# Optimization experiments

Hardware: AMD Instinct MI355X
Metric: run time of the kernel (lower is better)

## Reference

```python
import jax, jax.numpy as jnp
import numpy as np

B, NQ, NV = 4, 16384, 16384
DIM, FRAMES = 64, 4
D = DIM * FRAMES            # embed_dims = 256
HEADS, POINTS, LEVELS = 8, 4, 1
HD = D // HEADS             # head_dim = 32
HL, WL = 128, 128           # single-level feature map, HL*WL == NV
EPS = 1e-6


def setup_inputs() -> dict:
    key = jax.random.key(0)
    ks = jax.random.split(key, 14)
    inp = {
        "query": jax.random.normal(ks[0], (B, NQ, D), jnp.float32),
        "feat": jax.random.normal(ks[1], (B, NV, D), jnp.float32),
        "reference_points": jax.random.uniform(ks[2], (B, NQ, LEVELS, 2), jnp.float32),
        "spatial_shapes": jnp.array([[HL, WL]], jnp.int32),
        "level_start_index": jnp.array([0], jnp.int32),
        # LayerNorm params
        "qn_scale": jnp.ones((D,), jnp.float32),
        "qn_bias": jnp.zeros((D,), jnp.float32),
        "fn_scale": jnp.ones((D,), jnp.float32),
        "fn_bias": jnp.zeros((D,), jnp.float32),
        # MSDeformAttn projections
        "W_value": jax.random.normal(ks[3], (D, D), jnp.float32) / np.sqrt(D),
        "b_value": jnp.zeros((D,), jnp.float32),
        "W_off": jax.random.normal(ks[4], (D, HEADS * LEVELS * POINTS * 2), jnp.float32) * 0.01,
        "b_off": jax.random.normal(ks[5], (HEADS * LEVELS * POINTS * 2,), jnp.float32) * 0.5,
        "W_attn": jax.random.normal(ks[6], (D, HEADS * LEVELS * POINTS), jnp.float32) * 0.02,
        "b_attn": jnp.zeros((HEADS * LEVELS * POINTS,), jnp.float32),
        "W_out": jax.random.normal(ks[7], (D, D), jnp.float32) / np.sqrt(D),
        "b_out": jnp.zeros((D,), jnp.float32),
        # gamma is a learned scale (init 0 in the module; randomized here so it contributes)
        "gamma": jax.random.normal(ks[8], (D,), jnp.float32) * 0.1,
    }
    return inp


def _layer_norm(x, scale, bias):
    mu = jnp.mean(x, axis=-1, keepdims=True)
    var = jnp.mean(jnp.square(x - mu), axis=-1, keepdims=True)
    return (x - mu) * jax.lax.rsqrt(var + EPS) * scale + bias


def _bilinear_gather(v, loc, Hl, Wl):
    # v:   [B, H, N, hd] flattened level values (row-major HxW)
    # loc: [B, H, NQ, P, 2] normalized sampling locations in [0,1]
    # grid_sample semantics: align_corners=False, zero padding
    x = loc[..., 0] * Wl - 0.5
    y = loc[..., 1] * Hl - 0.5
    x0 = jnp.floor(x); y0 = jnp.floor(y)
    x1 = x0 + 1.0;     y1 = y0 + 1.0
    wx1 = x - x0; wx0 = 1.0 - wx1
    wy1 = y - y0; wy0 = 1.0 - wy1
    out = 0.0
    for xi, yi, w in ((x0, y0, wx0 * wy0), (x1, y0, wx1 * wy0),
                      (x0, y1, wx0 * wy1), (x1, y1, wx1 * wy1)):
        inb = (xi >= 0) & (xi < Wl) & (yi >= 0) & (yi < Hl)
        idx = (jnp.clip(yi, 0, Hl - 1) * Wl + jnp.clip(xi, 0, Wl - 1)).astype(jnp.int32)
        Bc, Hc, NQc, Pc = idx.shape
        g = jnp.take_along_axis(v, idx.reshape(Bc, Hc, NQc * Pc)[..., None], axis=2)
        g = g.reshape(Bc, Hc, NQc, Pc, -1)          # [B, H, NQ, P, hd]
        out = out + g * (w * inb)[..., None]
    return out


def reference(query, feat, reference_points, spatial_shapes, level_start_index,
              qn_scale, qn_bias, fn_scale, fn_bias,
              W_value, b_value, W_off, b_off, W_attn, b_attn, W_out, b_out, gamma):
    Bq, nq, _ = query.shape
    q = _layer_norm(query, qn_scale, qn_bias)
    v = _layer_norm(feat, fn_scale, fn_bias)

    # value projection -> per-head values [B, H, NV, hd]
    value = (v @ W_value + b_value).reshape(Bq, -1, HEADS, HD).transpose(0, 2, 1, 3)

    # sampling offsets [B, NQ, H, L, P, 2] and attention weights (softmax over L*P)
    off = (q @ W_off + b_off).reshape(Bq, nq, HEADS, LEVELS, POINTS, 2)
    aw = jax.nn.softmax((q @ W_attn + b_attn).reshape(Bq, nq, HEADS, LEVELS * POINTS), axis=-1)
    aw = aw.reshape(Bq, nq, HEADS, LEVELS, POINTS)

    ss = np.asarray(spatial_shapes)          # static level geometry
    lsi = np.asarray(level_start_index)
    offset_norm = ss[:, ::-1].astype(np.float32)  # (W, H) per level
    # sampling locations [B, NQ, H, L, P, 2]
    loc = reference_points[:, :, None, :, None, :] + off / offset_norm[None, None, None, :, None, :]

    acc = jnp.zeros((Bq, HEADS, nq, HD), query.dtype)
    for l in range(LEVELS):
        Hl, Wl = int(ss[l, 0]), int(ss[l, 1])
        start = int(lsi[l])
        v_l = value[:, :, start:start + Hl * Wl]                # [B, H, Hl*Wl, hd]
        loc_l = loc[:, :, :, l].transpose(0, 2, 1, 3, 4)        # [B, H, NQ, P, 2]
        sampled = _bilinear_gather(v_l, loc_l, Hl, Wl)          # [B, H, NQ, P, hd]
        aw_l = aw[:, :, :, l].transpose(0, 2, 1, 3)             # [B, H, NQ, P]
        acc = acc + jnp.einsum('bhnpd,bhnp->bhnd', sampled, aw_l)

    out = acc.transpose(0, 2, 1, 3).reshape(Bq, nq, D) @ W_out + b_out
    return query + gamma * out
```

## Files before the change

### kernel.cpp

```cpp
#include <hip/hip_runtime.h>

#define NQ 16384
#define NV 16384
#define DMODEL 256

typedef __bf16 bf16x8 __attribute__((ext_vector_type(8)));
typedef float f32x4 __attribute__((ext_vector_type(4)));

__device__ __forceinline__ unsigned short f2bf(float x) {
    union { float f; unsigned int u; } v; v.f = x;
    unsigned int r = v.u + 0x7fff + ((v.u >> 16) & 1);
    return (unsigned short)(r >> 16);
}
__device__ __forceinline__ float blo(unsigned int u) {
    union { unsigned int u; float f; } v; v.u = u << 16; return v.f;
}
__device__ __forceinline__ float bhi(unsigned int u) {
    union { unsigned int u; float f; } v; v.u = u & 0xFFFF0000u; return v.f;
}
__device__ __forceinline__ f32x4 mfma16(bf16x8 a, bf16x8 b, f32x4 c) {
    return __builtin_amdgcn_mfma_f32_16x16x32_bf16(a, b, c, 0, 0, 0);
}

__global__ __launch_bounds__(256) void k_prep(
    const float* __restrict__ Wv, const float* __restrict__ Woff,
    const float* __restrict__ Wattn, const float* __restrict__ Wout,
    unsigned short* __restrict__ WtV, unsigned short* __restrict__ WtC,
    unsigned short* __restrict__ WtO) {
    int t = blockIdx.x * 256 + threadIdx.x;
    if (t < 256 * 256) { int n = t >> 8, k = t & 255; WtV[t] = f2bf(Wv[k * 256 + n]); return; }
    t -= 256 * 256;
    if (t < 256 * 256) { int n = t >> 8, k = t & 255; WtO[t] = f2bf(Wout[k * 256 + n]); return; }
    t -= 256 * 256;
    if (t < 96 * 256) {
        int j = t >> 8, k = t & 255;
        float w = (j < 64) ? Woff[k * 64 + j] : Wattn[k * 32 + (j - 64)];
        WtC[j * 256 + k] = f2bf(w);
    }
}

__global__ __launch_bounds__(256) void k_ln(
    const float* __restrict__ feat, const float* __restrict__ query,
    const float* __restrict__ fns, const float* __restrict__ fnb,
    const float* __restrict__ qns, const float* __restrict__ qnb,
    unsigned short* __restrict__ lnf, unsigned short* __restrict__ lnq) {
    const int blk = blockIdx.x;
    const float* src; const float* scale; const float* bias; unsigned short* dst;
    int row0;
    if (blk < 2048) { src = feat;  scale = fns; bias = fnb; dst = lnf; row0 = blk * 32; }
    else            { src = query; scale = qns; bias = qnb; dst = lnq; row0 = (blk - 2048) * 32; }
    const int lane = threadIdx.x & 63;
    const int w = threadIdx.x >> 6;
    const int g = lane >> 4, li = lane & 15;
    float4 sc[4], bi[4];
#pragma unroll
    for (int j = 0; j < 4; ++j) {
        sc[j] = *(const float4*)(scale + li * 16 + j * 4);
        bi[j] = *(const float4*)(bias + li * 16 + j * 4);
    }
    const int r0 = row0 + w * 8 + g;
    float4 x[2][4];
#pragma unroll
    for (int h2 = 0; h2 < 2; ++h2)
#pragma unroll
        for (int j = 0; j < 4; ++j)
            x[h2][j] = *(const float4*)(src + (size_t)(r0 + h2 * 4) * 256 + li * 16 + j * 4);
#pragma unroll
    for (int h2 = 0; h2 < 2; ++h2) {
        float s = 0.f, sq = 0.f;
#pragma unroll
        for (int j = 0; j < 4; ++j) {
            s  += x[h2][j].x + x[h2][j].y + x[h2][j].z + x[h2][j].w;
            sq += x[h2][j].x * x[h2][j].x + x[h2][j].y * x[h2][j].y +
                  x[h2][j].z * x[h2][j].z + x[h2][j].w * x[h2][j].w;
        }
#pragma unroll
        for (int d = 1; d < 16; d <<= 1) {
            s  += __shfl_xor(s, d);
            sq += __shfl_xor(sq, d);
        }
        float mu = s * 0.00390625f;
        float rstd = rsqrtf(sq * 0.00390625f - mu * mu + 1e-6f);
        unsigned int pk[8];
#pragma unroll
        for (int j = 0; j < 4; ++j) {
            pk[2 * j] = (unsigned)f2bf((x[h2][j].x - mu) * rstd * sc[j].x + bi[j].x) |
                        ((unsigned)f2bf((x[h2][j].y - mu) * rstd * sc[j].y + bi[j].y) << 16);
            pk[2 * j + 1] = (unsigned)f2bf((x[h2][j].z - mu) * rstd * sc[j].z + bi[j].z) |
                            ((unsigned)f2bf((x[h2][j].w - mu) * rstd * sc[j].w + bi[j].w) << 16);
        }
        uint4* dstp = (uint4*)(dst + (size_t)(r0 + h2 * 4) * 256 + li * 16);
        dstp[0] = make_uint4(pk[0], pk[1], pk[2], pk[3]);
        dstp[1] = make_uint4(pk[4], pk[5], pk[6], pk[7]);
    }
}

#define STAGE_A(srcbuf)                                                               \
    {                                                                                 \
        const int c = threadIdx.x & 31;                                               \
        const int rt = threadIdx.x >> 5;                                              \
        _Pragma("unroll") for (int i = 0; i < 16; ++i) {                              \
            const int r = rt + i * 8;                                                 \
            *(uint4*)&A[r * 264 + c * 8] =                                            \
                *(const uint4*)((srcbuf) + (size_t)(m0 + r) * 256 + c * 8);           \
        }                                                                             \
    }

#define MFMA_STEP_V(bf, kk)                                                           \
    _Pragma("unroll") for (int m = 0; m < 8; ++m) {                                   \
        bf16x8 a = *(const bf16x8*)&A[(m * 16 + lrow) * 264 + (kk) * 32 + lk];        \
        _Pragma("unroll") for (int i = 0; i < 4; ++i)                                 \
            acc[i][m] = mfma16(bf[i], a, acc[i][m]);                                  \
    }

__global__ __launch_bounds__(256) void k_value(
    const unsigned short* __restrict__ lnf, const float* __restrict__ b_value,
    const unsigned short* __restrict__ WtV, unsigned short* __restrict__ value) {
    __shared__ unsigned short A[128 * 264];
    const int m0 = blockIdx.x * 128;
    STAGE_A(lnf)
    __syncthreads();
    const int lane = threadIdx.x & 63;
    const int w = threadIdx.x >> 6;
    const int lrow = lane & 15, lk = (lane >> 4) * 8;
    f32x4 acc[4][8];
#pragma unroll
    for (int i = 0; i < 4; ++i)
#pragma unroll
        for (int m = 0; m < 8; ++m) acc[i][m] = (f32x4){0.f, 0.f, 0.f, 0.f};
#define LOADB_V(dst, kk)                                                              \
    _Pragma("unroll") for (int i = 0; i < 4; ++i) dst[i] =                            \
        *(const bf16x8*)(WtV + (size_t)((w * 4 + i) * 16 + lrow) * 256 + (kk) * 32 + lk);
    {
        bf16x8 b0[4], b1[4];
        LOADB_V(b0, 0)
#pragma unroll
        for (int k2 = 0; k2 < 4; ++k2) {
            LOADB_V(b1, k2 * 2 + 1)
            MFMA_STEP_V(b0, k2 * 2)
            if (k2 < 3) { LOADB_V(b0, k2 * 2 + 2) }
            MFMA_STEP_V(b1, k2 * 2 + 1)
        }
    }
    const int g = lane >> 4;
    float4 bv[4];
#pragma unroll
    for (int i = 0; i < 4; ++i) bv[i] = *(const float4*)(b_value + (w * 4 + i) * 16 + g * 4);
#pragma unroll
    for (int m = 0; m < 8; ++m) {
        const size_t row = (size_t)(m0 + m * 16 + (lane & 15));
#pragma unroll
        for (int i = 0; i < 4; ++i) {
            const int col0 = (w * 4 + i) * 16 + g * 4;
            uint2 r;
            r.x = (unsigned)f2bf(acc[i][m][0] + bv[i].x) | ((unsigned)f2bf(acc[i][m][1] + bv[i].y) << 16);
            r.y = (unsigned)f2bf(acc[i][m][2] + bv[i].z) | ((unsigned)f2bf(acc[i][m][3] + bv[i].w) << 16);
            *(uint2*)(value + row * 256 + col0) = r;
        }
    }
}

__global__ __launch_bounds__(256) void k_qoff(
    const unsigned short* __restrict__ lnq, const float* __restrict__ refpt,
    const float* __restrict__ b_off, const float* __restrict__ b_attn,
    const unsigned short* __restrict__ WtC, float4* __restrict__ samples) {
    __shared__ unsigned short A[128 * 264];
    const int m0 = blockIdx.x * 128;
    STAGE_A(lnq)
    __syncthreads();
    const int lane = threadIdx.x & 63;
    const int w = threadIdx.x >> 6;
    const int lrow = lane & 15, lk = (lane >> 4) * 8;
    f32x4 acc[6][2];
#pragma unroll
    for (int i = 0; i < 6; ++i)
#pragma unroll
        for (int m = 0; m < 2; ++m) acc[i][m] = (f32x4){0.f, 0.f, 0.f, 0.f};
#define LOADB_Q(dst, kk)                                                              \
    _Pragma("unroll") for (int i = 0; i < 6; ++i) dst[i] =                            \
        *(const bf16x8*)(WtC + (size_t)(i * 16 + lrow) * 256 + (kk) * 32 + lk);
#define MFMA_STEP_Q(bf, kk)                                                           \
    _Pragma("unroll") for (int m = 0; m < 2; ++m) {                                   \
        bf16x8 a = *(const bf16x8*)&A[(w * 32 + m * 16 + lrow) * 264 + (kk) * 32 + lk]; \
        _Pragma("unroll") for (int i = 0; i < 6; ++i)                                 \
            acc[i][m] = mfma16(bf[i], a, acc[i][m]);                                  \
    }
    {
        bf16x8 b0[6], b1[6];
        LOADB_Q(b0, 0)
#pragma unroll
        for (int k2 = 0; k2 < 4; ++k2) {
            LOADB_Q(b1, k2 * 2 + 1)
            MFMA_STEP_Q(b0, k2 * 2)
            if (k2 < 3) { LOADB_Q(b0, k2 * 2 + 2) }
            MFMA_STEP_Q(b1, k2 * 2 + 1)
        }
    }
    __syncthreads();
    float* Dl = (float*)A + w * 4224;
#pragma unroll
    for (int i = 0; i < 6; ++i) {
        const int col0 = i * 16 + (lane >> 4) * 4;
#pragma unroll
        for (int m = 0; m < 2; ++m) {
            const int rl = m * 16 + (lane & 15);
            *(float4*)&Dl[rl * 100 + col0] =
                make_float4(acc[i][m][0], acc[i][m][1], acc[i][m][2], acc[i][m][3]);
        }
    }
    __syncthreads();
#pragma unroll
    for (int it = 0; it < 4; ++it) {
        int idx = it * 64 + lane;
        int rl = idx >> 3;
        int h = idx & 7;
        int row = m0 + w * 32 + rl;
        float rx = refpt[(size_t)row * 2 + 0] * 128.f - 0.5f;
        float ry = refpt[(size_t)row * 2 + 1] * 128.f - 0.5f;
        float l0 = Dl[rl * 100 + 64 + h * 4 + 0] + b_attn[h * 4 + 0];
        float l1 = Dl[rl * 100 + 64 + h * 4 + 1] + b_attn[h * 4 + 1];
        float l2 = Dl[rl * 100 + 64 + h * 4 + 2] + b_attn[h * 4 + 2];
        float l3 = Dl[rl * 100 + 64 + h * 4 + 3] + b_attn[h * 4 + 3];
        float mx = fmaxf(fmaxf(l0, l1), fmaxf(l2, l3));
        float e0 = __expf(l0 - mx), e1 = __expf(l1 - mx);
        float e2 = __expf(l2 - mx), e3 = __expf(l3 - mx);
        float inv = 1.f / (e0 + e1 + e2 + e3);
        float ww[4] = {e0 * inv, e1 * inv, e2 * inv, e3 * inv};
#pragma unroll
        for (int p = 0; p < 4; ++p) {
            float ox = Dl[rl * 100 + h * 8 + p * 2 + 0] + b_off[h * 8 + p * 2 + 0];
            float oy = Dl[rl * 100 + h * 8 + p * 2 + 1] + b_off[h * 8 + p * 2 + 1];
            samples[((size_t)row * 8 + h) * 4 + p] = make_float4(rx + ox, ry + oy, ww[p], 0.f);
        }
    }
}

__global__ __launch_bounds__(256) void k_gather(
    const unsigned short* __restrict__ value, const float4* __restrict__ samples,
    unsigned short* __restrict__ accb) {
    const int tid = blockIdx.x * 256 + threadIdx.x;
    const int sub = tid & 3;
    const int t = tid >> 2;
    const int h = t & 7;
    const int bq = t >> 3;
    const int b = bq >> 14;
    const unsigned short* vb = value + ((size_t)b << 14) * 256 + h * 32 + sub * 8;
    float a0 = 0.f, a1 = 0.f, a2 = 0.f, a3 = 0.f;
    float a4 = 0.f, a5 = 0.f, a6 = 0.f, a7 = 0.f;
#pragma unroll
    for (int p = 0; p < 4; ++p) {
        float4 s = samples[(size_t)t * 4 + p];
        float xf = floorf(s.x), yf = floorf(s.y);
        float fx = s.x - xf, fy = s.y - yf;
        int x0 = (int)xf, y0 = (int)yf;
        int x1 = x0 + 1, y1 = y0 + 1;
        float wgt = s.z;
        bool bx0 = (unsigned)x0 < 128u, bx1 = (unsigned)x1 < 128u;
        bool by0 = (unsigned)y0 < 128u, by1 = (unsigned)y1 < 128u;
        float wt[4];
        wt[0] = (bx0 && by0) ? (1.f - fx) * (1.f - fy) * wgt : 0.f;
        wt[1] = (bx1 && by0) ? fx * (1.f - fy) * wgt : 0.f;
        wt[2] = (bx0 && by1) ? (1.f - fx) * fy * wgt : 0.f;
        wt[3] = (bx1 && by1) ? fx * fy * wgt : 0.f;
        int xc0 = min(max(x0, 0), 127), xc1 = min(max(x1, 0), 127);
        int yc0 = min(max(y0, 0), 127), yc1 = min(max(y1, 0), 127);
        int pix[4];
        pix[0] = yc0 * 128 + xc0; pix[1] = yc0 * 128 + xc1;
        pix[2] = yc1 * 128 + xc0; pix[3] = yc1 * 128 + xc1;
#pragma unroll
        for (int tp = 0; tp < 4; ++tp) {
            uint4 u = *(const uint4*)(vb + (size_t)pix[tp] * 256);
            float w = wt[tp];
            a0 = fmaf(w, blo(u.x), a0); a1 = fmaf(w, bhi(u.x), a1);
            a2 = fmaf(w, blo(u.y), a2); a3 = fmaf(w, bhi(u.y), a3);
            a4 = fmaf(w, blo(u.z), a4); a5 = fmaf(w, bhi(u.z), a5);
            a6 = fmaf(w, blo(u.w), a6); a7 = fmaf(w, bhi(u.w), a7);
        }
    }
    uint4 r;
    r.x = (unsigned)f2bf(a0) | ((unsigned)f2bf(a1) << 16);
    r.y = (unsigned)f2bf(a2) | ((unsigned)f2bf(a3) << 16);
    r.z = (unsigned)f2bf(a4) | ((unsigned)f2bf(a5) << 16);
    r.w = (unsigned)f2bf(a6) | ((unsigned)f2bf(a7) << 16);
    *(uint4*)(accb + (size_t)bq * 256 + h * 32 + sub * 8) = r;
}

__global__ __launch_bounds__(256) void k_out(
    const unsigned short* __restrict__ accb, const unsigned short* __restrict__ WtO,
    const float* __restrict__ b_out, const float* __restrict__ gamma,
    const float* __restrict__ query, float* __restrict__ out) {
    __shared__ unsigned short A[128 * 264];
    const int m0 = blockIdx.x * 128;
    STAGE_A(accb)
    __syncthreads();
    const int lane = threadIdx.x & 63;
    const int w = threadIdx.x >> 6;
    const int lrow = lane & 15, lk = (lane >> 4) * 8;
    f32x4 acc[4][8];
#pragma unroll
    for (int i = 0; i < 4; ++i)
#pragma unroll
        for (int m = 0; m < 8; ++m) acc[i][m] = (f32x4){0.f, 0.f, 0.f, 0.f};
#define LOADB_O(dst, kk)                                                              \
    _Pragma("unroll") for (int i = 0; i < 4; ++i) dst[i] =                            \
        *(const bf16x8*)(WtO + (size_t)((w * 4 + i) * 16 + lrow) * 256 + (kk) * 32 + lk);
    {
        bf16x8 b0[4], b1[4];
        LOADB_O(b0, 0)
#pragma unroll
        for (int k2 = 0; k2 < 4; ++k2) {
            LOADB_O(b1, k2 * 2 + 1)
            MFMA_STEP_V(b0, k2 * 2)
            if (k2 < 3) { LOADB_O(b0, k2 * 2 + 2) }
            MFMA_STEP_V(b1, k2 * 2 + 1)
        }
    }
    const int g = lane >> 4;
    float4 bo[4], gm[4];
#pragma unroll
    for (int i = 0; i < 4; ++i) {
        bo[i] = *(const float4*)(b_out + (w * 4 + i) * 16 + g * 4);
        gm[i] = *(const float4*)(gamma + (w * 4 + i) * 16 + g * 4);
    }
#pragma unroll
    for (int m = 0; m < 8; ++m) {
        const size_t row = (size_t)(m0 + m * 16 + (lane & 15));
#pragma unroll
        for (int i = 0; i < 4; ++i) {
            const int col0 = (w * 4 + i) * 16 + g * 4;
            float4 q = *(const float4*)(query + row * 256 + col0);
            float4 o;
            o.x = q.x + gm[i].x * (acc[i][m][0] + bo[i].x);
            o.y = q.y + gm[i].y * (acc[i][m][1] + bo[i].y);
            o.z = q.z + gm[i].z * (acc[i][m][2] + bo[i].z);
            o.w = q.w + gm[i].w * (acc[i][m][3] + bo[i].w);
            *(float4*)(out + row * 256 + col0) = o;
        }
    }
}

extern "C" void kernel_launch(void* const* d_in, const int* in_sizes, int n_in,
                              void* d_out, int out_size, void* d_ws, size_t ws_size,
                              hipStream_t stream) {
    const float* query    = (const float*)d_in[0];
    const float* feat     = (const float*)d_in[1];
    const float* refpt    = (const float*)d_in[2];
    const float* qn_scale = (const float*)d_in[5];
    const float* qn_bias  = (const float*)d_in[6];
    const float* fn_scale = (const float*)d_in[7];
    const float* fn_bias  = (const float*)d_in[8];
    const float* W_value  = (const float*)d_in[9];
    const float* b_value  = (const float*)d_in[10];
    const float* W_off    = (const float*)d_in[11];
    const float* b_off    = (const float*)d_in[12];
    const float* W_attn   = (const float*)d_in[13];
    const float* b_attn   = (const float*)d_in[14];
    const float* W_out    = (const float*)d_in[15];
    const float* b_out    = (const float*)d_in[16];
    const float* gamma    = (const float*)d_in[17];
    float* out = (float*)d_out;

    char* ws = (char*)d_ws;
    unsigned short* WtV   = (unsigned short*)(ws);
    unsigned short* WtO   = (unsigned short*)(ws + 131072);
    unsigned short* WtC   = (unsigned short*)(ws + 262144);
    unsigned short* value = (unsigned short*)(ws + 311296);
    char* regA = ws + 311296 + 33554432;
    char* regB = ws + 311296 + 2 * 33554432;
    unsigned short* lnf     = (unsigned short*)regA;
    float4*         samples = (float4*)regA;
    unsigned short* lnq     = (unsigned short*)regB;
    unsigned short* accb    = (unsigned short*)regB;

    hipLaunchKernelGGL(k_prep, dim3(608), dim3(256), 0, stream,
                       W_value, W_off, W_attn, W_out, WtV, WtC, WtO);
    hipLaunchKernelGGL(k_ln, dim3(4096), dim3(256), 0, stream,
                       feat, query, fn_scale, fn_bias, qn_scale, qn_bias, lnf, lnq);
    hipLaunchKernelGGL(k_value, dim3(512), dim3(256), 0, stream,
                       lnf, b_value, WtV, value);
    hipLaunchKernelGGL(k_qoff, dim3(512), dim3(256), 0, stream,
                       lnq, refpt, b_off, b_attn, WtC, samples);
    hipLaunchKernelGGL(k_gather, dim3(8192), dim3(256), 0, stream,
                       value, samples, accb);
    hipLaunchKernelGGL(k_out, dim3(512), dim3(256), 0, stream,
                       accb, WtO, b_out, gamma, query, out);
}
```

Measured before the change: 190.9 us.

## Merge weight prep into LayerNorm kernel and stage value-projection stores through LDS

Weight transposition and both LayerNorms now run in a single launch, which removes one kernel boundary. Each LN block handles 128 rows instead of 32, with double-buffered register loads so the next rows' loads overlap the current rows' normalization. The value GEMM epilogue writes its bf16 results to shared memory first and then stores full coalesced 16-byte rows, replacing scattered 8-byte global stores. The cost is two extra barriers, higher register pressure in the LN kernel, and fewer LN blocks.

```diff
diff --git a/kernel.cpp b/kernel.cpp
--- a/kernel.cpp
+++ b/kernel.cpp
@@ -22,33 +22,33 @@
     return __builtin_amdgcn_mfma_f32_16x16x32_bf16(a, b, c, 0, 0, 0);
 }
 
-__global__ __launch_bounds__(256) void k_prep(
+__global__ __launch_bounds__(256) void k_prep_ln(
     const float* __restrict__ Wv, const float* __restrict__ Woff,
     const float* __restrict__ Wattn, const float* __restrict__ Wout,
     unsigned short* __restrict__ WtV, unsigned short* __restrict__ WtC,
-    unsigned short* __restrict__ WtO) {
-    int t = blockIdx.x * 256 + threadIdx.x;
-    if (t < 256 * 256) { int n = t >> 8, k = t & 255; WtV[t] = f2bf(Wv[k * 256 + n]); return; }
-    t -= 256 * 256;
-    if (t < 256 * 256) { int n = t >> 8, k = t & 255; WtO[t] = f2bf(Wout[k * 256 + n]); return; }
-    t -= 256 * 256;
-    if (t < 96 * 256) {
-        int j = t >> 8, k = t & 255;
-        float w = (j < 64) ? Woff[k * 64 + j] : Wattn[k * 32 + (j - 64)];
-        WtC[j * 256 + k] = f2bf(w);
-    }
-}
-
-__global__ __launch_bounds__(256) void k_ln(
+    unsigned short* __restrict__ WtO,
     const float* __restrict__ feat, const float* __restrict__ query,
     const float* __restrict__ fns, const float* __restrict__ fnb,
     const float* __restrict__ qns, const float* __restrict__ qnb,
     unsigned short* __restrict__ lnf, unsigned short* __restrict__ lnq) {
-    const int blk = blockIdx.x;
+    if (blockIdx.x < 608) {
+        int t = blockIdx.x * 256 + threadIdx.x;
+        if (t < 256 * 256) { int n = t >> 8, k = t & 255; WtV[t] = f2bf(Wv[k * 256 + n]); return; }
+        t -= 256 * 256;
+        if (t < 256 * 256) { int n = t >> 8, k = t & 255; WtO[t] = f2bf(Wout[k * 256 + n]); return; }
+        t -= 256 * 256;
+        if (t < 96 * 256) {
+            int j = t >> 8, k = t & 255;
+            float w = (j < 64) ? Woff[k * 64 + j] : Wattn[k * 32 + (j - 64)];
+            WtC[j * 256 + k] = f2bf(w);
+        }
+        return;
+    }
+    const int lb = blockIdx.x - 608;
     const float* src; const float* scale; const float* bias; unsigned short* dst;
     int row0;
-    if (blk < 2048) { src = feat;  scale = fns; bias = fnb; dst = lnf; row0 = blk * 32; }
-    else            { src = query; scale = qns; bias = qnb; dst = lnq; row0 = (blk - 2048) * 32; }
+    if (lb < 512) { src = feat;  scale = fns; bias = fnb; dst = lnf; row0 = lb * 128; }
+    else          { src = query; scale = qns; bias = qnb; dst = lnq; row0 = (lb - 512) * 128; }
     const int lane = threadIdx.x & 63;
     const int w = threadIdx.x >> 6;
     const int g = lane >> 4, li = lane & 15;
@@ -58,41 +58,46 @@
         sc[j] = *(const float4*)(scale + li * 16 + j * 4);
         bi[j] = *(const float4*)(bias + li * 16 + j * 4);
     }
-    const int r0 = row0 + w * 8 + g;
-    float4 x[2][4];
-#pragma unroll
-    for (int h2 = 0; h2 < 2; ++h2)
-#pragma unroll
-        for (int j = 0; j < 4; ++j)
-            x[h2][j] = *(const float4*)(src + (size_t)(r0 + h2 * 4) * 256 + li * 16 + j * 4);
-#pragma unroll
-    for (int h2 = 0; h2 < 2; ++h2) {
-        float s = 0.f, sq = 0.f;
-#pragma unroll
-        for (int j = 0; j < 4; ++j) {
-            s  += x[h2][j].x + x[h2][j].y + x[h2][j].z + x[h2][j].w;
-            sq += x[h2][j].x * x[h2][j].x + x[h2][j].y * x[h2][j].y +
-                  x[h2][j].z * x[h2][j].z + x[h2][j].w * x[h2][j].w;
-        }
-#pragma unroll
-        for (int d = 1; d < 16; d <<= 1) {
-            s  += __shfl_xor(s, d);
-            sq += __shfl_xor(sq, d);
-        }
-        float mu = s * 0.00390625f;
-        float rstd = rsqrtf(sq * 0.00390625f - mu * mu + 1e-6f);
-        unsigned int pk[8];
-#pragma unroll
-        for (int j = 0; j < 4; ++j) {
-            pk[2 * j] = (unsigned)f2bf((x[h2][j].x - mu) * rstd * sc[j].x + bi[j].x) |
-                        ((unsigned)f2bf((x[h2][j].y - mu) * rstd * sc[j].y + bi[j].y) << 16);
-            pk[2 * j + 1] = (unsigned)f2bf((x[h2][j].z - mu) * rstd * sc[j].z + bi[j].z) |
-                            ((unsigned)f2bf((x[h2][j].w - mu) * rstd * sc[j].w + bi[j].w) << 16);
-        }
-        uint4* dstp = (uint4*)(dst + (size_t)(r0 + h2 * 4) * 256 + li * 16);
-        dstp[0] = make_uint4(pk[0], pk[1], pk[2], pk[3]);
-        dstp[1] = make_uint4(pk[4], pk[5], pk[6], pk[7]);
-    }
+    const int rbase = row0 + w * 8 + g;
+
+    float4 xa[2][4], xb[2][4];
+#define LN_LOAD(buf, coff)                                                            \
+    _Pragma("unroll") for (int h2 = 0; h2 < 2; ++h2)                                  \
+        _Pragma("unroll") for (int j = 0; j < 4; ++j)                                 \
+            buf[h2][j] = *(const float4*)(src + (size_t)(rbase + (coff) + h2 * 4) * 256 + li * 16 + j * 4);
+#define LN_PROC(buf, coff)                                                            \
+    _Pragma("unroll") for (int h2 = 0; h2 < 2; ++h2) {                                \
+        float s = 0.f, sq = 0.f;                                                      \
+        _Pragma("unroll") for (int j = 0; j < 4; ++j) {                               \
+            s  += buf[h2][j].x + buf[h2][j].y + buf[h2][j].z + buf[h2][j].w;          \
+            sq += buf[h2][j].x * buf[h2][j].x + buf[h2][j].y * buf[h2][j].y +         \
+                  buf[h2][j].z * buf[h2][j].z + buf[h2][j].w * buf[h2][j].w;          \
+        }                                                                             \
+        _Pragma("unroll") for (int d = 1; d < 16; d <<= 1) {                          \
+            s  += __shfl_xor(s, d);                                                   \
+            sq += __shfl_xor(sq, d);                                                  \
+        }                                                                             \
+        float mu = s * 0.00390625f;                                                   \
+        float rstd = rsqrtf(sq * 0.00390625f - mu * mu + 1e-6f);                      \
+        unsigned int pk[8];                                                           \
+        _Pragma("unroll") for (int j = 0; j < 4; ++j) {                               \
+            pk[2 * j] = (unsigned)f2bf((buf[h2][j].x - mu) * rstd * sc[j].x + bi[j].x) |      \
+                        ((unsigned)f2bf((buf[h2][j].y - mu) * rstd * sc[j].y + bi[j].y) << 16); \
+            pk[2 * j + 1] = (unsigned)f2bf((buf[h2][j].z - mu) * rstd * sc[j].z + bi[j].z) |   \
+                            ((unsigned)f2bf((buf[h2][j].w - mu) * rstd * sc[j].w + bi[j].w) << 16); \
+        }                                                                             \
+        uint4* dstp = (uint4*)(dst + (size_t)(rbase + (coff) + h2 * 4) * 256 + li * 16); \
+        dstp[0] = make_uint4(pk[0], pk[1], pk[2], pk[3]);                             \
+        dstp[1] = make_uint4(pk[4], pk[5], pk[6], pk[7]);                             \
+    }
+    LN_LOAD(xa, 0)
+    LN_LOAD(xb, 32)
+    LN_PROC(xa, 0)
+    LN_LOAD(xa, 64)
+    LN_PROC(xb, 32)
+    LN_LOAD(xb, 96)
+    LN_PROC(xa, 64)
+    LN_PROC(xb, 96)
 }
 
 #define STAGE_A(srcbuf)                                                               \
@@ -142,20 +147,28 @@
             MFMA_STEP_V(b1, k2 * 2 + 1)
         }
     }
+    __syncthreads();
     const int g = lane >> 4;
-    float4 bv[4];
-#pragma unroll
-    for (int i = 0; i < 4; ++i) bv[i] = *(const float4*)(b_value + (w * 4 + i) * 16 + g * 4);
-#pragma unroll
-    for (int m = 0; m < 8; ++m) {
-        const size_t row = (size_t)(m0 + m * 16 + (lane & 15));
-#pragma unroll
-        for (int i = 0; i < 4; ++i) {
-            const int col0 = (w * 4 + i) * 16 + g * 4;
+#pragma unroll
+    for (int i = 0; i < 4; ++i) {
+        const int col0 = (w * 4 + i) * 16 + g * 4;
+        float4 bv = *(const float4*)(b_value + col0);
+#pragma unroll
+        for (int m = 0; m < 8; ++m) {
             uint2 r;
-            r.x = (unsigned)f2bf(acc[i][m][0] + bv[i].x) | ((unsigned)f2bf(acc[i][m][1] + bv[i].y) << 16);
-            r.y = (unsigned)f2bf(acc[i][m][2] + bv[i].z) | ((unsigned)f2bf(acc[i][m][3] + bv[i].w) << 16);
-            *(uint2*)(value + row * 256 + col0) = r;
+            r.x = (unsigned)f2bf(acc[i][m][0] + bv.x) | ((unsigned)f2bf(acc[i][m][1] + bv.y) << 16);
+            r.y = (unsigned)f2bf(acc[i][m][2] + bv.z) | ((unsigned)f2bf(acc[i][m][3] + bv.w) << 16);
+            *(uint2*)&A[(m * 16 + (lane & 15)) * 264 + col0] = r;
+        }
+    }
+    __syncthreads();
+    {
+        const int c = threadIdx.x & 31;
+        const int rt = threadIdx.x >> 5;
+#pragma unroll
+        for (int i = 0; i < 16; ++i) {
+            const int r = rt + i * 8;
+            *(uint4*)(value + (size_t)(m0 + r) * 256 + c * 8) = *(uint4*)&A[r * 264 + c * 8];
         }
     }
 }
@@ -372,9 +385,8 @@
     unsigned short* lnq     = (unsigned short*)regB;
     unsigned short* accb    = (unsigned short*)regB;
 
-    hipLaunchKernelGGL(k_prep, dim3(608), dim3(256), 0, stream,
-                       W_value, W_off, W_attn, W_out, WtV, WtC, WtO);
-    hipLaunchKernelGGL(k_ln, dim3(4096), dim3(256), 0, stream,
+    hipLaunchKernelGGL(k_prep_ln, dim3(1632), dim3(256), 0, stream,
+                       W_value, W_off, W_attn, W_out, WtV, WtC, WtO,
                        feat, query, fn_scale, fn_bias, qn_scale, qn_bias, lnf, lnq);
     hipLaunchKernelGGL(k_value, dim3(512), dim3(256), 0, stream,
                        lnf, b_value, WtV, value);
```

Result: no change. 191.4 us (+0.3%).
